# Kernel optimization log

Hardware: AMD Instinct MI355X
Metric: run time of the kernel (lower is better)

## Reference

```python
import jax, jax.numpy as jnp
import numpy as np

H = 896          # hidden_size
S = H // 2       # split_size = 448
Q = 256          # quantisation
B = 16384        # batch (parallel sampling streams)


def setup_inputs() -> dict:
    key = jax.random.key(0)
    ks = jax.random.split(key, 16)
    sc = 0.02
    return {
        "prev_y": jax.random.uniform(ks[0], (B, 2), dtype=jnp.float32),
        "prev_hidden": jax.random.normal(ks[1], (B, H), dtype=jnp.float32),
        "current_coarse": jax.random.uniform(ks[2], (B, 1), dtype=jnp.float32),
        # torch Linear weights are [out_features, in_features]
        "R_w": sc * jax.random.normal(ks[3], (3 * H, H), dtype=jnp.float32),
        "Ic_w": sc * jax.random.normal(ks[4], (3 * S, 2), dtype=jnp.float32),
        "If_w": sc * jax.random.normal(ks[5], (3 * S, 3), dtype=jnp.float32),
        "bias_u": jnp.zeros((H,), jnp.float32),
        "bias_r": jnp.zeros((H,), jnp.float32),
        "bias_e": jnp.zeros((H,), jnp.float32),
        "O1_w": sc * jax.random.normal(ks[6], (S, S), dtype=jnp.float32),
        "O1_b": jnp.zeros((S,), jnp.float32),
        "O2_w": sc * jax.random.normal(ks[7], (Q, S), dtype=jnp.float32),
        "O2_b": jnp.zeros((Q,), jnp.float32),
        "O3_w": sc * jax.random.normal(ks[8], (S, S), dtype=jnp.float32),
        "O3_b": jnp.zeros((S,), jnp.float32),
        "O4_w": sc * jax.random.normal(ks[9], (Q, S), dtype=jnp.float32),
        "O4_b": jnp.zeros((Q,), jnp.float32),
    }


def reference(prev_y, prev_hidden, current_coarse,
              R_w, Ic_w, If_w, bias_u, bias_r, bias_e,
              O1_w, O1_b, O2_w, O2_b, O3_w, O3_b, O4_w, O4_b):
    # recurrent projection: [B,H] @ [H,3H] -> [B,3H]
    R_hidden = prev_hidden @ R_w.T
    R_u, R_r, R_e = jnp.split(R_hidden, 3, axis=1)

    # coarse input projection: [B,2] -> [B,3S]
    cproj = prev_y @ Ic_w.T
    Ic_u, Ic_r, Ic_e = jnp.split(cproj, 3, axis=1)

    # fine input projection: [B,3] -> [B,3S]
    fine_in = jnp.concatenate([prev_y, current_coarse], axis=1)
    fproj = fine_in @ If_w.T
    If_u, If_r, If_e = jnp.split(fproj, 3, axis=1)

    I_u = jnp.concatenate([Ic_u, If_u], axis=1)  # [B,H]
    I_r = jnp.concatenate([Ic_r, If_r], axis=1)
    I_e = jnp.concatenate([Ic_e, If_e], axis=1)

    u = jax.nn.sigmoid(R_u + I_u + bias_u)
    r = jax.nn.sigmoid(R_r + I_r + bias_r)
    e = jnp.tanh(r * R_e + I_e + bias_e)
    hidden = u * prev_hidden + (1.0 - u) * e  # [B,H]

    h_coarse, h_fine = jnp.split(hidden, 2, axis=1)  # [B,S] each
    out_coarse = jax.nn.relu(h_coarse @ O1_w.T + O1_b) @ O2_w.T + O2_b  # [B,Q]
    out_fine = jax.nn.relu(h_fine @ O3_w.T + O3_b) @ O4_w.T + O4_b      # [B,Q]
    return (out_coarse, out_fine, hidden)
```

## Files before the change

### kernel.cpp

```cpp
#include <hip/hip_runtime.h>
#include <hip/hip_bf16.h>
#include <cstdint>

#define BB 16384
#define HH 896
#define SS 448
#define QQ 256
#define NPAD 2816

typedef __attribute__((ext_vector_type(4))) float f32x4;
typedef __attribute__((ext_vector_type(8))) short bf16x8;

__device__ __forceinline__ short f2bf(float f){
  union { float f; uint32_t u; } x; x.f = f;
  uint32_t r = (x.u + 0x7fffu + ((x.u >> 16) & 1u)) >> 16;
  return (short)r;
}
__device__ __forceinline__ float bf2f(short b){
  union { uint32_t u; float f; } x; x.u = ((uint32_t)(uint16_t)b) << 16;
  return x.f;
}

__global__ void cast4_kernel(const float* __restrict__ src, short* __restrict__ dst, long n4){
  long i = (long)blockIdx.x * blockDim.x + threadIdx.x;
  if (i >= n4) return;
  const float4 v = reinterpret_cast<const float4*>(src)[i];
  short4 o; o.x = f2bf(v.x); o.y = f2bf(v.y); o.z = f2bf(v.z); o.w = f2bf(v.w);
  reinterpret_cast<short4*>(dst)[i] = o;
}

__global__ void castpad_kernel(const float* __restrict__ src, short* __restrict__ dst,
                               int srows, int scols, int dcols, int total){
  int i = blockIdx.x * blockDim.x + threadIdx.x;
  if (i >= total) return;
  int r = i / dcols, c = i - r * dcols;
  float v = (r < srows && c < scols) ? src[(long)r * scols + c] : 0.f;
  dst[i] = f2bf(v);
}

__global__ __launch_bounds__(512, 2)
void gemm256_bt(const short* __restrict__ A, int lda,
                const short* __restrict__ Bt, int ldb,
                short* __restrict__ C, int ldc, int Nvalid,
                int K, int nbn)
{
  __shared__ short smem[65536];
  const int tid = threadIdx.x;
  const int w  = tid >> 6, ln = tid & 63;
  const int wr = w >> 2,  wc = w & 3;
  const int lr = ln & 15;
  const int lg = ln >> 4;
  const int srow = ln >> 3;
  const int sgc  = (ln & 7) ^ srow;

  int wg = blockIdx.x;
  const int cpx = gridDim.x >> 3;
  wg = (wg & 7) * cpx + (wg >> 3);
  const int bm = wg / nbn, bn = wg - bm * nbn;
  const long m0 = (long)bm * 256, n0 = (long)bn * 256;

  f32x4 acc[8][4] = {};

  auto stage = [&](const short* __restrict__ src, int ld, long rbase, int k0,
                   int lbase , int h) {
#pragma unroll
    for (int i = 0; i < 2; ++i) {
      const int rloc = h * 128 + i * 64 + w * 8;
      const short* g = src + (rbase + rloc + srow) * (long)ld + k0 + sgc * 8;
      __builtin_amdgcn_global_load_lds(
          (const __attribute__((address_space(1))) void*)g,
          (__attribute__((address_space(3))) void*)&smem[lbase + rloc * 64],
          16, 0, 0);
    }
  };
  auto rd = [&](int lbase, int r, int ks) -> bf16x8 {
    const int gc = ks * 4 + lg;
    return *reinterpret_cast<const bf16x8*>(&smem[lbase + r * 64 + ((gc ^ (r & 7)) << 3)]);
  };

  const int NT = K >> 6;
  stage(Bt, ldb, n0, 0, 32768, 0);
  stage(Bt, ldb, n0, 0, 32768, 1);
  stage(A,  lda, m0, 0, 0,     0);
  stage(A,  lda, m0, 0, 0,     1);
  asm volatile("s_waitcnt vmcnt(2)" ::: "memory");
  __builtin_amdgcn_s_barrier();
  asm volatile("" ::: "memory");
  __builtin_amdgcn_sched_barrier(0);

  for (int j = 0; j < NT; ++j) {
    const int Ab = (j & 1) * 16384;
    const int Bb = 32768 + (j & 1) * 16384;
    const int An = ((j + 1) & 1) * 16384;
    const int Bn = 32768 + ((j + 1) & 1) * 16384;
    const bool pf = (j + 1 < NT);
    const int k1 = (j + 1) << 6;
    bf16x8 b[4][2];
#pragma unroll
    for (int q = 0; q < 4; ++q) {
      bf16x8 a[2][2];
#pragma unroll
      for (int dm = 0; dm < 2; ++dm)
#pragma unroll
        for (int ks = 0; ks < 2; ++ks)
          a[dm][ks] = rd(Ab, q * 64 + dm * 32 + wr * 16 + lr, ks);
      if (q == 0) {
#pragma unroll
        for (int n = 0; n < 4; ++n)
#pragma unroll
          for (int ks = 0; ks < 2; ++ks)
            b[n][ks] = rd(Bb, wc * 64 + n * 16 + lr, ks);
      }
      if (pf) {
        if      (q == 0) stage(Bt, ldb, n0, k1, Bn, 0);
        else if (q == 1) stage(Bt, ldb, n0, k1, Bn, 1);
        else if (q == 2) stage(A,  lda, m0, k1, An, 0);
        else             stage(A,  lda, m0, k1, An, 1);
      }
      asm volatile("" ::: "memory");
      __builtin_amdgcn_s_barrier();
      asm volatile("s_waitcnt lgkmcnt(0)" ::: "memory");
      __builtin_amdgcn_sched_barrier(0);
      __builtin_amdgcn_s_setprio(1);
#pragma unroll
      for (int dm = 0; dm < 2; ++dm)
#pragma unroll
        for (int n = 0; n < 4; ++n)
#pragma unroll
          for (int ks = 0; ks < 2; ++ks)
            acc[2 * q + dm][n] = __builtin_amdgcn_mfma_f32_16x16x32_bf16(
                a[dm][ks], b[n][ks], acc[2 * q + dm][n], 0, 0, 0);
      __builtin_amdgcn_s_setprio(0);
      __builtin_amdgcn_sched_barrier(0);
      if (q == 1) {
        if (pf) asm volatile("s_waitcnt vmcnt(4)" ::: "memory");
        else    asm volatile("s_waitcnt vmcnt(0)" ::: "memory");
      } else if (q == 3) {
        asm volatile("s_waitcnt vmcnt(2)" ::: "memory");
      }
      asm volatile("" ::: "memory");
      __builtin_amdgcn_s_barrier();
      asm volatile("" ::: "memory");
      __builtin_amdgcn_sched_barrier(0);
    }
  }

  const int lc = ln & 15, rg = lg * 4;
#pragma unroll
  for (int n = 0; n < 4; ++n) {
    long col = n0 + wc * 64 + n * 16 + lc;
    if (col < Nvalid) {
#pragma unroll
      for (int m = 0; m < 8; ++m) {
        long row = m0 + m * 32 + wr * 16 + rg;
#pragma unroll
        for (int reg = 0; reg < 4; ++reg)
          C[(row + reg) * (long)ldc + col] = f2bf(acc[m][n][reg]);
      }
    }
  }
}

#define EP_RELU_BIAS_BF16 1
#define EP_BIAS_F32 2

template<int EP>
__global__ __launch_bounds__(256)
void gemm_bt(const short* __restrict__ A0, const short* __restrict__ A1, int lda,
             const short* __restrict__ W0, const short* __restrict__ W1, int ldb,
             void* __restrict__ C0v, void* __restrict__ C1v, int ldc,
             const float* __restrict__ bias0, const float* __restrict__ bias1, int nbias,
             int K)
{
  const short* A  = blockIdx.z ? A1 : A0;
  const short* Bt = blockIdx.z ? W1 : W0;
  void* Cv        = blockIdx.z ? C1v : C0v;
  const float* bias = blockIdx.z ? bias1 : bias0;

  __shared__ short As[128 * 64];
  __shared__ short Bs[128 * 64];
  const int tid = threadIdx.x;
  const int wv = tid >> 6, ln = tid & 63;
  const int wr = wv >> 1, wc = wv & 1;
  const long m0 = (long)blockIdx.y * 128;
  const long n0 = (long)blockIdx.x * 128;

  f32x4 acc[4][4] = {};
  const int lr = ln & 15;
  const int lkbase = (ln >> 4) * 8;
  const int e0 = ln * 8;
  for (int k0 = 0; k0 < K; k0 += 64) {
    __syncthreads();
#pragma unroll
    for (int i = 0; i < 4; i++) {
      int chunk = wv * 4 + i;
      int e = chunk * 512 + e0;
      int row = e >> 6, col = e & 63;
      const short* g = A + (m0 + row) * lda + k0 + col;
      __builtin_amdgcn_global_load_lds((const __attribute__((address_space(1))) void*)g,
                                       (__attribute__((address_space(3))) void*)&As[chunk * 512],
                                       16, 0, 0);
    }
#pragma unroll
    for (int i = 0; i < 4; i++) {
      int chunk = wv * 4 + i;
      int e = chunk * 512 + e0;
      int row = e >> 6, col = e & 63;
      const short* g = Bt + (n0 + row) * ldb + k0 + col;
      __builtin_amdgcn_global_load_lds((const __attribute__((address_space(1))) void*)g,
                                       (__attribute__((address_space(3))) void*)&Bs[chunk * 512],
                                       16, 0, 0);
    }
    __syncthreads();
#pragma unroll
    for (int ks = 0; ks < 2; ks++) {
      bf16x8 a[4], b[4];
#pragma unroll
      for (int m = 0; m < 4; m++)
        a[m] = *reinterpret_cast<const bf16x8*>(&As[(wr * 64 + m * 16 + lr) * 64 + ks * 32 + lkbase]);
#pragma unroll
      for (int n = 0; n < 4; n++)
        b[n] = *reinterpret_cast<const bf16x8*>(&Bs[(wc * 64 + n * 16 + lr) * 64 + ks * 32 + lkbase]);
#pragma unroll
      for (int m = 0; m < 4; m++)
#pragma unroll
        for (int n = 0; n < 4; n++)
          acc[m][n] = __builtin_amdgcn_mfma_f32_16x16x32_bf16(a[m], b[n], acc[m][n], 0, 0, 0);
    }
  }

  const int lc = ln & 15;
  const int r4 = (ln >> 4) * 4;
#pragma unroll
  for (int m = 0; m < 4; m++) {
#pragma unroll
    for (int n = 0; n < 4; n++) {
      long col = n0 + wc * 64 + n * 16 + lc;
#pragma unroll
      for (int reg = 0; reg < 4; reg++) {
        long row = m0 + wr * 64 + m * 16 + r4 + reg;
        float v = acc[m][n][reg];
        if (EP == EP_RELU_BIAS_BF16) {
          float bv = (col < nbias) ? bias[col] : 0.f;
          v += bv;
          v = v > 0.f ? v : 0.f;
          ((short*)Cv)[row * ldc + col] = f2bf(v);
        } else {
          v += bias[col];
          ((float*)Cv)[row * ldc + col] = v;
        }
      }
    }
  }
}

__global__ void gates_kernel(const float* __restrict__ prev_y,
                             const float* __restrict__ prev_hidden,
                             const float* __restrict__ ccoarse,
                             const float* __restrict__ Icw,
                             const float* __restrict__ Ifw,
                             const float* __restrict__ bu,
                             const float* __restrict__ br,
                             const float* __restrict__ be,
                             const short* __restrict__ Rh,
                             float* __restrict__ hid_out,
                             short* __restrict__ hid_bf)
{
  const int b = blockIdx.y;
  const int h = blockIdx.x * 128 + threadIdx.x;
  const float py0 = prev_y[2 * b], py1 = prev_y[2 * b + 1], c0 = ccoarse[b];
  float iu, ir, ie;
  if (h < SS) {
    int j = h;
    iu = py0 * Icw[2 * j]            + py1 * Icw[2 * j + 1];
    ir = py0 * Icw[2 * (SS + j)]     + py1 * Icw[2 * (SS + j) + 1];
    ie = py0 * Icw[2 * (2 * SS + j)] + py1 * Icw[2 * (2 * SS + j) + 1];
  } else {
    int j = h - SS;
    iu = py0 * Ifw[3 * j]            + py1 * Ifw[3 * j + 1]            + c0 * Ifw[3 * j + 2];
    ir = py0 * Ifw[3 * (SS + j)]     + py1 * Ifw[3 * (SS + j) + 1]     + c0 * Ifw[3 * (SS + j) + 2];
    ie = py0 * Ifw[3 * (2 * SS + j)] + py1 * Ifw[3 * (2 * SS + j) + 1] + c0 * Ifw[3 * (2 * SS + j) + 2];
  }
  const long base = (long)b * (3 * HH);
  float ru = bf2f(Rh[base + h]);
  float rr = bf2f(Rh[base + HH + h]);
  float re = bf2f(Rh[base + 2 * HH + h]);
  float u = 1.f / (1.f + __expf(-(ru + iu + bu[h])));
  float r = 1.f / (1.f + __expf(-(rr + ir + br[h])));
  float e = tanhf(r * re + ie + be[h]);
  float ph = prev_hidden[(long)b * HH + h];
  float hd = u * ph + (1.f - u) * e;
  hid_out[(long)b * HH + h] = hd;
  hid_bf[(long)b * HH + h] = f2bf(hd);
}

extern "C" void kernel_launch(void* const* d_in, const int* in_sizes, int n_in,
                              void* d_out, int out_size, void* d_ws, size_t ws_size,
                              hipStream_t stream)
{
  (void)in_sizes; (void)n_in; (void)out_size; (void)ws_size;
  const float* prev_y      = (const float*)d_in[0];
  const float* prev_hidden = (const float*)d_in[1];
  const float* ccoarse     = (const float*)d_in[2];
  const float* R_w  = (const float*)d_in[3];
  const float* Ic_w = (const float*)d_in[4];
  const float* If_w = (const float*)d_in[5];
  const float* bu   = (const float*)d_in[6];
  const float* br   = (const float*)d_in[7];
  const float* be   = (const float*)d_in[8];
  const float* O1w  = (const float*)d_in[9];
  const float* O1b  = (const float*)d_in[10];
  const float* O2w  = (const float*)d_in[11];
  const float* O2b  = (const float*)d_in[12];
  const float* O3w  = (const float*)d_in[13];
  const float* O3b  = (const float*)d_in[14];
  const float* O4w  = (const float*)d_in[15];
  const float* O4b  = (const float*)d_in[16];

  float* out_coarse = (float*)d_out;
  float* out_fine   = out_coarse + (long)BB * QQ;
  float* hidden     = out_fine + (long)BB * QQ;

  char* ws = (char*)d_ws;
  short* Ah   = (short*)(ws + 0);
  short* Rwh  = (short*)(ws + 29360128);
  short* Rh   = (short*)(ws + 34406400);
  short* hidb = (short*)(ws + 122486784);
  short* O1wb = (short*)(ws + 151846912);
  short* O3wb = (short*)(ws + 152305664);
  short* O2wb = (short*)(ws + 152764416);
  short* O4wb = (short*)(ws + 153026560);
  short* t1   = (short*)(ws + 0);
  short* t2   = (short*)(ws + 16777216);

  long nAh4 = (long)BB * HH / 4;
  cast4_kernel<<<(int)((nAh4 + 255) / 256), 256, 0, stream>>>(prev_hidden, Ah, nAh4);
  castpad_kernel<<<(NPAD * HH + 255) / 256, 256, 0, stream>>>(R_w, Rwh, 3 * HH, HH, HH, NPAD * HH);
  castpad_kernel<<<(512 * 448 + 255) / 256, 256, 0, stream>>>(O1w, O1wb, 448, 448, 448, 512 * 448);
  castpad_kernel<<<(512 * 448 + 255) / 256, 256, 0, stream>>>(O3w, O3wb, 448, 448, 448, 512 * 448);
  castpad_kernel<<<(256 * 512 + 255) / 256, 256, 0, stream>>>(O2w, O2wb, 256, 448, 512, 256 * 512);
  castpad_kernel<<<(256 * 512 + 255) / 256, 256, 0, stream>>>(O4w, O4wb, 256, 448, 512, 256 * 512);

  gemm256_bt<<<(BB / 256) * (NPAD / 256), 512, 0, stream>>>(
      Ah, HH, Rwh, HH, Rh, 3 * HH, 3 * HH, HH, NPAD / 256);

  gates_kernel<<<dim3(7, BB), 128, 0, stream>>>(prev_y, prev_hidden, ccoarse,
                                                Ic_w, If_w, bu, br, be, Rh, hidden, hidb);

  gemm_bt<EP_RELU_BIAS_BF16><<<dim3(4, BB / 128, 2), 256, 0, stream>>>(
      hidb, hidb + 448, HH, O1wb, O3wb, 448, t1, t2, 512, O1b, O3b, 448, 448);
  gemm_bt<EP_BIAS_F32><<<dim3(2, BB / 128, 2), 256, 0, stream>>>(
      t1, t2, 512, O2wb, O4wb, 512, out_coarse, out_fine, 256, O2b, O4b, 256, 512);
}
```

Before: 268.2 us.

## Vectorize gates kernel, merge output-weight casts, reorder GEMM staging

The gates kernel now has each thread handle 8 consecutive hidden units, using 16-byte vector loads and stores for Rh, prev_hidden, the biases and the outputs. The old version used one thread per element with scalar 2-byte loads. The four small output-weight cast launches are merged into one kernel to cut launch overhead. The big GEMM's prefetch order is also changed so that one A half-tile is staged first and the B halves in between. This may change whether the vmcnt(2) wait covers the data needed for the first iteration, which is a correctness risk.

```diff
diff --git a/kernel.cpp b/kernel.cpp
--- a/kernel.cpp
+++ b/kernel.cpp
@@ -36,6 +36,23 @@
   int r = i / dcols, c = i - r * dcols;
   float v = (r < srows && c < scols) ? src[(long)r * scols + c] : 0.f;
   dst[i] = f2bf(v);
+}
+
+__global__ void castpadO_kernel(const float* __restrict__ O1w, const float* __restrict__ O3w,
+                                const float* __restrict__ O2w, const float* __restrict__ O4w,
+                                short* __restrict__ O1b, short* __restrict__ O3b,
+                                short* __restrict__ O2b, short* __restrict__ O4b){
+  int i = blockIdx.x * 256 + threadIdx.x;
+  const int n13 = 512 * 448, n24 = 256 * 512;
+  const float* src; short* dst; int srows, scols, dcols, j;
+  if (i < n13)                { src = O1w; dst = O1b; srows = 448; scols = 448; dcols = 448; j = i; }
+  else if (i < 2 * n13)       { src = O3w; dst = O3b; srows = 448; scols = 448; dcols = 448; j = i - n13; }
+  else if (i < 2 * n13 + n24) { src = O2w; dst = O2b; srows = 256; scols = 448; dcols = 512; j = i - 2 * n13; }
+  else if (i < 2 * (n13 + n24)) { src = O4w; dst = O4b; srows = 256; scols = 448; dcols = 512; j = i - 2 * n13 - n24; }
+  else return;
+  int r = j / dcols, c = j - r * dcols;
+  float v = (r < srows && c < scols) ? src[(long)r * scols + c] : 0.f;
+  dst[j] = f2bf(v);
 }
 
 __global__ __launch_bounds__(512, 2)
@@ -79,9 +96,9 @@
   };
 
   const int NT = K >> 6;
+  stage(A,  lda, m0, 0, 0,     0);
   stage(Bt, ldb, n0, 0, 32768, 0);
   stage(Bt, ldb, n0, 0, 32768, 1);
-  stage(A,  lda, m0, 0, 0,     0);
   stage(A,  lda, m0, 0, 0,     1);
   asm volatile("s_waitcnt vmcnt(2)" ::: "memory");
   __builtin_amdgcn_s_barrier();
@@ -112,9 +129,9 @@
             b[n][ks] = rd(Bb, wc * 64 + n * 16 + lr, ks);
       }
       if (pf) {
-        if      (q == 0) stage(Bt, ldb, n0, k1, Bn, 0);
-        else if (q == 1) stage(Bt, ldb, n0, k1, Bn, 1);
-        else if (q == 2) stage(A,  lda, m0, k1, An, 0);
+        if      (q == 0) stage(A,  lda, m0, k1, An, 0);
+        else if (q == 1) stage(Bt, ldb, n0, k1, Bn, 0);
+        else if (q == 2) stage(Bt, ldb, n0, k1, Bn, 1);
         else             stage(A,  lda, m0, k1, An, 1);
       }
       asm volatile("" ::: "memory");
@@ -254,44 +271,80 @@
   }
 }
 
-__global__ void gates_kernel(const float* __restrict__ prev_y,
-                             const float* __restrict__ prev_hidden,
-                             const float* __restrict__ ccoarse,
-                             const float* __restrict__ Icw,
-                             const float* __restrict__ Ifw,
-                             const float* __restrict__ bu,
-                             const float* __restrict__ br,
-                             const float* __restrict__ be,
-                             const short* __restrict__ Rh,
-                             float* __restrict__ hid_out,
-                             short* __restrict__ hid_bf)
+__global__ __launch_bounds__(256)
+void gates_kernel(const float* __restrict__ prev_y,
+                  const float* __restrict__ prev_hidden,
+                  const float* __restrict__ ccoarse,
+                  const float* __restrict__ Icw,
+                  const float* __restrict__ Ifw,
+                  const float* __restrict__ bu,
+                  const float* __restrict__ br,
+                  const float* __restrict__ be,
+                  const short* __restrict__ Rh,
+                  float* __restrict__ hid_out,
+                  short* __restrict__ hid_bf)
 {
-  const int b = blockIdx.y;
-  const int h = blockIdx.x * 128 + threadIdx.x;
+  const int v = blockIdx.x * 256 + threadIdx.x;
+  const int b = v / 112;
+  const int h0 = (v - b * 112) * 8;
+  const long rbase = (long)b * (3 * HH);
+
+  const bf16x8 ru8 = *reinterpret_cast<const bf16x8*>(Rh + rbase + h0);
+  const bf16x8 rr8 = *reinterpret_cast<const bf16x8*>(Rh + rbase + HH + h0);
+  const bf16x8 re8 = *reinterpret_cast<const bf16x8*>(Rh + rbase + 2 * HH + h0);
+  const float4* ph4 = reinterpret_cast<const float4*>(prev_hidden + (long)b * HH + h0);
+  const float4 pha = ph4[0], phb = ph4[1];
   const float py0 = prev_y[2 * b], py1 = prev_y[2 * b + 1], c0 = ccoarse[b];
-  float iu, ir, ie;
-  if (h < SS) {
-    int j = h;
-    iu = py0 * Icw[2 * j]            + py1 * Icw[2 * j + 1];
-    ir = py0 * Icw[2 * (SS + j)]     + py1 * Icw[2 * (SS + j) + 1];
-    ie = py0 * Icw[2 * (2 * SS + j)] + py1 * Icw[2 * (2 * SS + j) + 1];
+
+  float iu[8], ir[8], ie[8];
+  if (h0 < SS) {
+    const float4* cu = reinterpret_cast<const float4*>(Icw + 2 * h0);
+    const float4* cr = reinterpret_cast<const float4*>(Icw + 2 * (SS + h0));
+    const float4* ce = reinterpret_cast<const float4*>(Icw + 2 * (2 * SS + h0));
+#pragma unroll
+    for (int q = 0; q < 4; ++q) {
+      float4 a = cu[q]; iu[2*q] = py0*a.x + py1*a.y; iu[2*q+1] = py0*a.z + py1*a.w;
+      float4 r = cr[q]; ir[2*q] = py0*r.x + py1*r.y; ir[2*q+1] = py0*r.z + py1*r.w;
+      float4 e = ce[q]; ie[2*q] = py0*e.x + py1*e.y; ie[2*q+1] = py0*e.z + py1*e.w;
+    }
   } else {
-    int j = h - SS;
-    iu = py0 * Ifw[3 * j]            + py1 * Ifw[3 * j + 1]            + c0 * Ifw[3 * j + 2];
-    ir = py0 * Ifw[3 * (SS + j)]     + py1 * Ifw[3 * (SS + j) + 1]     + c0 * Ifw[3 * (SS + j) + 2];
-    ie = py0 * Ifw[3 * (2 * SS + j)] + py1 * Ifw[3 * (2 * SS + j) + 1] + c0 * Ifw[3 * (2 * SS + j) + 2];
-  }
-  const long base = (long)b * (3 * HH);
-  float ru = bf2f(Rh[base + h]);
-  float rr = bf2f(Rh[base + HH + h]);
-  float re = bf2f(Rh[base + 2 * HH + h]);
-  float u = 1.f / (1.f + __expf(-(ru + iu + bu[h])));
-  float r = 1.f / (1.f + __expf(-(rr + ir + br[h])));
-  float e = tanhf(r * re + ie + be[h]);
-  float ph = prev_hidden[(long)b * HH + h];
-  float hd = u * ph + (1.f - u) * e;
-  hid_out[(long)b * HH + h] = hd;
-  hid_bf[(long)b * HH + h] = f2bf(hd);
+    const int j0 = h0 - SS;
+    const float* fu = Ifw + 3 * j0;
+    const float* fr = Ifw + 3 * (SS + j0);
+    const float* fe = Ifw + 3 * (2 * SS + j0);
+#pragma unroll
+    for (int j = 0; j < 8; ++j) {
+      iu[j] = py0 * fu[3*j] + py1 * fu[3*j+1] + c0 * fu[3*j+2];
+      ir[j] = py0 * fr[3*j] + py1 * fr[3*j+1] + c0 * fr[3*j+2];
+      ie[j] = py0 * fe[3*j] + py1 * fe[3*j+1] + c0 * fe[3*j+2];
+    }
+  }
+  const float4* bu4 = reinterpret_cast<const float4*>(bu + h0);
+  const float4* br4 = reinterpret_cast<const float4*>(br + h0);
+  const float4* be4 = reinterpret_cast<const float4*>(be + h0);
+  float buv[8], brv[8], bev[8];
+  { float4 a = bu4[0], b2 = bu4[1];
+    buv[0]=a.x; buv[1]=a.y; buv[2]=a.z; buv[3]=a.w; buv[4]=b2.x; buv[5]=b2.y; buv[6]=b2.z; buv[7]=b2.w; }
+  { float4 a = br4[0], b2 = br4[1];
+    brv[0]=a.x; brv[1]=a.y; brv[2]=a.z; brv[3]=a.w; brv[4]=b2.x; brv[5]=b2.y; brv[6]=b2.z; brv[7]=b2.w; }
+  { float4 a = be4[0], b2 = be4[1];
+    bev[0]=a.x; bev[1]=a.y; bev[2]=a.z; bev[3]=a.w; bev[4]=b2.x; bev[5]=b2.y; bev[6]=b2.z; bev[7]=b2.w; }
+  float ph[8] = { pha.x, pha.y, pha.z, pha.w, phb.x, phb.y, phb.z, phb.w };
+
+  float hd[8];
+  bf16x8 hb;
+#pragma unroll
+  for (int j = 0; j < 8; ++j) {
+    float u = 1.f / (1.f + __expf(-(bf2f(ru8[j]) + iu[j] + buv[j])));
+    float r = 1.f / (1.f + __expf(-(bf2f(rr8[j]) + ir[j] + brv[j])));
+    float e = tanhf(r * bf2f(re8[j]) + ie[j] + bev[j]);
+    hd[j] = u * ph[j] + (1.f - u) * e;
+    hb[j] = f2bf(hd[j]);
+  }
+  float4* ho = reinterpret_cast<float4*>(hid_out + (long)b * HH + h0);
+  ho[0] = make_float4(hd[0], hd[1], hd[2], hd[3]);
+  ho[1] = make_float4(hd[4], hd[5], hd[6], hd[7]);
+  *reinterpret_cast<bf16x8*>(hid_bf + (long)b * HH + h0) = hb;
 }
 
 extern "C" void kernel_launch(void* const* d_in, const int* in_sizes, int n_in,
@@ -336,16 +389,14 @@
   long nAh4 = (long)BB * HH / 4;
   cast4_kernel<<<(int)((nAh4 + 255) / 256), 256, 0, stream>>>(prev_hidden, Ah, nAh4);
   castpad_kernel<<<(NPAD * HH + 255) / 256, 256, 0, stream>>>(R_w, Rwh, 3 * HH, HH, HH, NPAD * HH);
-  castpad_kernel<<<(512 * 448 + 255) / 256, 256, 0, stream>>>(O1w, O1wb, 448, 448, 448, 512 * 448);
-  castpad_kernel<<<(512 * 448 + 255) / 256, 256, 0, stream>>>(O3w, O3wb, 448, 448, 448, 512 * 448);
-  castpad_kernel<<<(256 * 512 + 255) / 256, 256, 0, stream>>>(O2w, O2wb, 256, 448, 512, 256 * 512);
-  castpad_kernel<<<(256 * 512 + 255) / 256, 256, 0, stream>>>(O4w, O4wb, 256, 448, 512, 256 * 512);
+  castpadO_kernel<<<(2 * (512 * 448 + 256 * 512) + 255) / 256, 256, 0, stream>>>(
+      O1w, O3w, O2w, O4w, O1wb, O3wb, O2wb, O4wb);
 
   gemm256_bt<<<(BB / 256) * (NPAD / 256), 512, 0, stream>>>(
       Ah, HH, Rwh, HH, Rh, 3 * HH, 3 * HH, HH, NPAD / 256);
 
-  gates_kernel<<<dim3(7, BB), 128, 0, stream>>>(prev_y, prev_hidden, ccoarse,
-                                                Ic_w, If_w, bu, br, be, Rh, hidden, hidb);
+  gates_kernel<<<BB * 112 / 256, 256, 0, stream>>>(prev_y, prev_hidden, ccoarse,
+                                                   Ic_w, If_w, bu, br, be, Rh, hidden, hidb);
 
   gemm_bt<EP_RELU_BIAS_BF16><<<dim3(4, BB / 128, 2), 256, 0, stream>>>(
       hidb, hidb + 448, HH, O1wb, O3wb, 448, t1, t2, 512, O1b, O3b, 448, 448);
```

Result: faster. 254.2 us (-5.2%).
